# Performance work log

Hardware: AMD Instinct MI355X
Metric: run time of the kernel (lower is better)

The kernel has to match this reference:

```python
import jax, jax.numpy as jnp
import numpy as np

D = 1024      # input_dim
H = 4096      # hidden_dim
E = 8         # expert_count
TOP_K = 2
N = 8192      # tokens
LN_EPS = 1e-5


def setup_inputs() -> dict:
    key = jax.random.key(0)
    ks = jax.random.split(key, 10)
    s_d = 1.0 / np.sqrt(D)
    s_h = 1.0 / np.sqrt(H)
    return {
        "x": jax.random.normal(ks[0], (N, D), dtype=jnp.float32),
        "ln_gamma": jnp.ones((D,), jnp.float32),
        "ln_beta": jnp.zeros((D,), jnp.float32),
        "conf_w": jax.random.uniform(ks[1], (D, 1), jnp.float32, -s_d, s_d),
        "conf_b": jnp.zeros((1,), jnp.float32),
        "router_w": jax.random.uniform(ks[2], (D, E), jnp.float32, -s_d, s_d),
        "router_b": jnp.zeros((E,), jnp.float32),
        "w1": jax.random.uniform(ks[3], (E, D, H), jnp.float32, -s_d, s_d),
        "b1": jax.random.uniform(ks[4], (E, H), jnp.float32, -s_d, s_d),
        "w2": jax.random.uniform(ks[5], (E, H, D), jnp.float32, -s_h, s_h),
        "b2": jax.random.uniform(ks[6], (E, D), jnp.float32, -s_h, s_h),
    }


def reference(x, ln_gamma, ln_beta, conf_w, conf_b, router_w, router_b, w1, b1, w2, b2):
    # LayerNorm (torch default eps=1e-5, affine)
    mu = jnp.mean(x, axis=-1, keepdims=True)
    var = jnp.mean(jnp.square(x - mu), axis=-1, keepdims=True)
    x_norm = (x - mu) * jax.lax.rsqrt(var + LN_EPS) * ln_gamma + ln_beta

    # layer-skip confidence head
    confidence = jax.nn.sigmoid(x_norm @ conf_w + conf_b)  # [N,1]

    # router: softmax -> top-k -> renormalize selected weights
    router_probs = jax.nn.softmax(x_norm @ router_w + router_b, axis=-1)  # [N,E]
    vals, indices = jax.lax.top_k(router_probs, TOP_K)                    # [N,K]
    vals = vals / jnp.sum(vals, axis=-1, keepdims=True)

    # scatter top-k weights into dense per-expert combine weights [N,E]
    combine_w = jnp.zeros((x.shape[0], E), x.dtype).at[
        jnp.arange(x.shape[0])[:, None], indices].add(vals)

    # dispatch/combine: loop over small fixed expert count (dense compute,
    # weighted by combine_w, mathematically identical to per-token dispatch)
    combined = jnp.zeros_like(x)
    for e in range(E):
        h = jax.nn.relu(x_norm @ w1[e] + b1[e])      # [N,H]
        combined = combined + combine_w[:, e:e + 1] * (h @ w2[e] + b2[e])

    output = x + combined
    return output, confidence, x
```

## Files before the change

kernel.cpp:

```cpp
#include <hip/hip_runtime.h>
#include <hip/hip_bf16.h>

#define N_TOK 8192
#define DIM   1024
#define HID   4096
#define NEXP  8
#define CSTR  64
#define RTMAX 136
#define HROWS 16896
#define EPS   264

using bf16x8 = __attribute__((ext_vector_type(8))) short;
using f32x4  = __attribute__((ext_vector_type(4))) float;

__device__ __forceinline__ void gload_lds16(const void* g, void* l) {
  __builtin_amdgcn_global_load_lds(
      (const __attribute__((address_space(1))) unsigned int*)g,
      (__attribute__((address_space(3))) unsigned int*)l, 16, 0, 0);
}

__device__ __forceinline__ float wredsum(float v) {
#pragma unroll
  for (int off = 32; off > 0; off >>= 1) v += __shfl_xor(v, off, 64);
  return v;
}

__device__ __forceinline__ unsigned short f2bf(float f) {
  __hip_bfloat16 h = __float2bfloat16(f);
  return *reinterpret_cast<unsigned short*>(&h);
}
__device__ __forceinline__ float bf2f(unsigned short u) {
  return __uint_as_float((unsigned)u << 16);
}

__device__ __forceinline__ void transpose_body(
    const float* __restrict__ src, __hip_bfloat16* __restrict__ dst,
    int R, int C, int c0, int r0, float (*tile)[65]) {
  const int tid = threadIdx.x;
  const int tx = tid & 15, ty = tid >> 4;
#pragma unroll
  for (int k = 0; k < 4; k++) {
    const int row = ty + k * 16;
    const float4 v = *(const float4*)(src + (size_t)(r0 + row) * C + c0 + tx * 4);
    tile[row][tx * 4 + 0] = v.x; tile[row][tx * 4 + 1] = v.y;
    tile[row][tx * 4 + 2] = v.z; tile[row][tx * 4 + 3] = v.w;
  }
  __syncthreads();
#pragma unroll
  for (int k = 0; k < 4; k++) {
    const int orow = ty + k * 16;
    ushort4 st;
    st.x = f2bf(tile[tx * 4 + 0][orow]);
    st.y = f2bf(tile[tx * 4 + 1][orow]);
    st.z = f2bf(tile[tx * 4 + 2][orow]);
    st.w = f2bf(tile[tx * 4 + 3][orow]);
    *(ushort4*)((unsigned short*)dst + (size_t)(c0 + orow) * R + r0 + tx * 4) = st;
  }
}

__global__ __launch_bounds__(256) void setup_kernel(
    const float* __restrict__ x, const float* __restrict__ gamma, const float* __restrict__ beta,
    const float* __restrict__ conf_w, const float* __restrict__ conf_b,
    const float* __restrict__ rw, const float* __restrict__ rb,
    const float* __restrict__ w1, const float* __restrict__ w2,
    __hip_bfloat16* __restrict__ w1t, __hip_bfloat16* __restrict__ w2t,
    __hip_bfloat16* __restrict__ xn, float* __restrict__ out,
    int* __restrict__ counts, int* __restrict__ lists, float* __restrict__ wts,
    int2* __restrict__ idx) {
  __shared__ float tile[64][65];
  const int b = (int)blockIdx.x;
  if (b < 8192) {
    const int z = b >> 10, r = b & 1023;
    const int cx = r & 63, ry = r >> 6;
    transpose_body(w1 + (size_t)z * DIM * HID, w1t + (size_t)z * DIM * HID,
                   DIM, HID, cx * 64, ry * 64, tile);
    return;
  }
  if (b < 16384) {
    const int bb = b - 8192;
    const int z = bb >> 10, r = bb & 1023;
    const int cx = r & 15, ry = r >> 4;
    transpose_body(w2 + (size_t)z * HID * DIM, w2t + (size_t)z * HID * DIM,
                   HID, DIM, cx * 64, ry * 64, tile);
    return;
  }
  const int t = (b - 16384) * 4 + ((int)threadIdx.x >> 6);
  const int lane = threadIdx.x & 63;
  const float* xr = x + (size_t)t * DIM;

  float4 xv[4];
#pragma unroll
  for (int q = 0; q < 4; q++) xv[q] = *(const float4*)(xr + q * 256 + lane * 4);

  float s = 0.f, s2 = 0.f;
#pragma unroll
  for (int q = 0; q < 4; q++) {
    s  += xv[q].x + xv[q].y + xv[q].z + xv[q].w;
    s2 += xv[q].x * xv[q].x + xv[q].y * xv[q].y + xv[q].z * xv[q].z + xv[q].w * xv[q].w;
  }
  s = wredsum(s); s2 = wredsum(s2);
  const float mu  = s * (1.f / DIM);
  const float inv = rsqrtf(s2 * (1.f / DIM) - mu * mu + 1e-5f);

  float p[9];
#pragma unroll
  for (int e = 0; e < 9; e++) p[e] = 0.f;

#pragma unroll
  for (int q = 0; q < 4; q++) {
    const int d0 = q * 256 + lane * 4;
    const float4 g4 = *(const float4*)(gamma + d0);
    const float4 b4 = *(const float4*)(beta + d0);
    float v0 = (xv[q].x - mu) * inv * g4.x + b4.x;
    float v1 = (xv[q].y - mu) * inv * g4.y + b4.y;
    float v2 = (xv[q].z - mu) * inv * g4.z + b4.z;
    float v3 = (xv[q].w - mu) * inv * g4.w + b4.w;

    ushort4 st; st.x = f2bf(v0); st.y = f2bf(v1); st.z = f2bf(v2); st.w = f2bf(v3);
    *(ushort4*)((unsigned short*)xn + (size_t)t * DIM + d0) = st;
    *(float4*)(out + (size_t)t * DIM + d0) = xv[q];
    *(float4*)(out + (size_t)N_TOK * DIM + N_TOK + (size_t)t * DIM + d0) = xv[q];

    const float vv[4] = {v0, v1, v2, v3};
#pragma unroll
    for (int j = 0; j < 4; j++) {
      const int d = d0 + j;
      const float v = vv[j];
      p[8] += v * conf_w[d];
      const float4 r0 = *(const float4*)(rw + d * 8);
      const float4 r1 = *(const float4*)(rw + d * 8 + 4);
      p[0] += v * r0.x; p[1] += v * r0.y; p[2] += v * r0.z; p[3] += v * r0.w;
      p[4] += v * r1.x; p[5] += v * r1.y; p[6] += v * r1.z; p[7] += v * r1.w;
    }
  }
#pragma unroll
  for (int e = 0; e < 9; e++) p[e] = wredsum(p[e]);

  if (lane == 0) {
    float L[8];
#pragma unroll
    for (int e = 0; e < 8; e++) L[e] = p[e] + rb[e];
    const float cl = p[8] + conf_b[0];
    out[(size_t)N_TOK * DIM + t] = 1.f / (1.f + expf(-cl));

    float mx = L[0];
#pragma unroll
    for (int e = 1; e < 8; e++) mx = fmaxf(mx, L[e]);
    float pe[8];
#pragma unroll
    for (int e = 0; e < 8; e++) pe[e] = expf(L[e] - mx);
    int i0 = 0; float v0 = pe[0];
#pragma unroll
    for (int e = 1; e < 8; e++) if (pe[e] > v0) { v0 = pe[e]; i0 = e; }
    int i1 = -1; float v1 = -1.f;
#pragma unroll
    for (int e = 0; e < 8; e++) if (e != i0 && pe[e] > v1) { v1 = pe[e]; i1 = e; }
    const float wsum = v0 + v1;
    const float w0 = v0 / wsum, w1v = v1 / wsum;
    int p0 = atomicAdd(&counts[i0 * CSTR], 1);
    lists[i0 * N_TOK + p0] = t; wts[i0 * N_TOK + p0] = w0;
    int p1 = atomicAdd(&counts[i1 * CSTR], 1);
    lists[i1 * N_TOK + p1] = t; wts[i1 * N_TOK + p1] = w1v;
    idx[t] = make_int2((i0 << 13) | p0, (i1 << 13) | p1);
  }
}

__global__ void bases_kernel(const int* __restrict__ counts, int* __restrict__ bases,
                             int* __restrict__ meta) {
  if (threadIdx.x == 0) {
    int s = 0, r = 0;
#pragma unroll
    for (int e = 0; e < NEXP; e++) {
      bases[e] = s; meta[e] = r;
      const int c = counts[e * CSTR];
      s += c; r += (c + 127) >> 7;
    }
    meta[NEXP] = r;
  }
}


#define LGKM_SB(N)                                                            \
  asm volatile("s_waitcnt lgkmcnt(" #N ")" ::: "memory");                     \
  __builtin_amdgcn_sched_barrier(0);

#define MFMA_G(MI, N0, NN)                                                    \
  __builtin_amdgcn_s_setprio(1);                                              \
  _Pragma("unroll")                                                           \
  for (int n = (N0); n < (N0) + (NN); n++)                                    \
    acc[MI][n] = __builtin_amdgcn_mfma_f32_16x16x32_bf16(afr[MI], bfr[n], acc[MI][n], 0, 0, 0); \
  __builtin_amdgcn_s_setprio(0);

#define GEMM_CORE(NT)                                                                   \
  f32x4 acc[4][4] = {};                                                                 \
  stage(0, 0); stage(1, 24576);                                                         \
  for (int t = 0; t < (NT); ++t) {                                                      \
    const int pb = (t % 3) * 24576;                                                     \
    if (t + 1 < (NT)) { asm volatile("s_waitcnt vmcnt(3)" ::: "memory"); }              \
    else              { asm volatile("s_waitcnt vmcnt(0)" ::: "memory"); }              \
    __builtin_amdgcn_s_barrier();                                                       \
    if (t + 2 < (NT)) stage(t + 2, ((t + 2) % 3) * 24576);                              \
    const char* Ab = smem + pb + Abase;                                                 \
    const char* Bb = smem + pb + Bbase;                                                 \
    bf16x8 bfr[4], afr[4];                                                              \
    afr[0] = *(const bf16x8*)(Ab);                                                      \
    bfr[0] = *(const bf16x8*)(Bb);                                                      \
    bfr[1] = *(const bf16x8*)(Bb + 1024);                                               \
    __builtin_amdgcn_sched_barrier(0);                                                  \
    bfr[2] = *(const bf16x8*)(Bb + 2048);                                               \
    __builtin_amdgcn_sched_barrier(0);                                                  \
    bfr[3] = *(const bf16x8*)(Bb + 3072);                                               \
    __builtin_amdgcn_sched_barrier(0);                                                  \
    afr[1] = *(const bf16x8*)(Ab + 1024);                                               \
    __builtin_amdgcn_sched_barrier(0);                                                  \
    afr[2] = *(const bf16x8*)(Ab + 2048);                                               \
    __builtin_amdgcn_sched_barrier(0);                                                  \
    afr[3] = *(const bf16x8*)(Ab + 3072);                                               \
    __builtin_amdgcn_sched_barrier(0);                                                  \
    LGKM_SB(5) MFMA_G(0, 0, 2)                                                          \
    LGKM_SB(4) MFMA_G(0, 2, 1)                                                          \
    LGKM_SB(3) MFMA_G(0, 3, 1)                                                          \
    LGKM_SB(2) MFMA_G(1, 0, 4)                                                          \
    LGKM_SB(1) MFMA_G(2, 0, 4)                                                          \
    LGKM_SB(0) MFMA_G(3, 0, 4)                                                          \
  }

#define DECODE_TAIL()                                                         \
  if (rtg >= meta[NEXP]) return;                                              \
  int e = 0;                                                                  \
  _Pragma("unroll")                                                           \
  for (int k = 1; k < NEXP; k++) if (meta[k] <= rtg) e = k;                   \
  const int rt = rtg - meta[e];                                               \
  const int cnt = counts[e * CSTR];                                           \
  const int hbase = bases[e];

#define GEMM_COMMON()                                                         \
  __shared__ char smem[73728];                                                \
  const int tid = threadIdx.x;                                                \
  const int l = tid & 63;                                                     \
  const int w8 = tid >> 6;                                                    \
  const int wr = w8 >> 2;                                                     \
  const int wc = w8 & 3;                                                      \
  const int lr = l & 15;                                                      \
  const int pchunk = (l >> 4) ^ ((lr >> 1) & 3);                              \
  const int Abase = (wr * 64 + lr) * 64 + pchunk * 16;                        \
  const int Bbase = 8192 + (wc * 64 + lr) * 64 + pchunk * 16;                 \
  const int srow = tid >> 2;                                                  \
  const int lc = (tid & 3) ^ ((srow >> 1) & 3);

#define EPILOGUE(DSTROW)                                                      \
  __builtin_amdgcn_s_barrier();                                               \
  {                                                                           \
    unsigned short* ep = (unsigned short*)smem;                               \
    _Pragma("unroll")                                                         \
    for (int n = 0; n < 4; n++) {                                             \
      const int col = wc * 64 + n * 16 + lr;                                  \
      _Pragma("unroll")                                                       \
      for (int m = 0; m < 4; m++) {                                           \
        f32x4 v = acc[m][n];                                                  \
        _Pragma("unroll")                                                     \
        for (int j = 0; j < 4; j++) {                                         \
          const int row = wr * 64 + m * 16 + (l >> 4) * 4 + j;                \
          ep[row * EPS + col] = f2bf(v[j]);                                   \
        }                                                                     \
      }                                                                       \
    }                                                                         \
    asm volatile("s_waitcnt lgkmcnt(0)" ::: "memory");                        \
    __builtin_amdgcn_s_barrier();                                             \
    const int g = tid >> 5, u = tid & 31;                                     \
    _Pragma("unroll")                                                         \
    for (int i = 0; i < 8; i++) {                                             \
      const int row = i * 16 + g;                                             \
      const int pos = rt * 128 + row;                                         \
      if (pos < cnt) {                                                        \
        bf16x8 vv = *(const bf16x8*)(ep + row * EPS + u * 8);                 \
        *(bf16x8*)(DSTROW + u * 8) = vv;                                      \
      }                                                                       \
    }                                                                         \
  }

__global__ __launch_bounds__(512, 4) void gemm1_kernel(
    const __hip_bfloat16* __restrict__ xn, const __hip_bfloat16* __restrict__ w1t_b,
    const float* __restrict__ b1, const int* __restrict__ lists,
    const int* __restrict__ counts, const int* __restrict__ bases,
    const int* __restrict__ meta, __hip_bfloat16* __restrict__ hbuf) {
  const int x_ = (int)blockIdx.x & 7;
  const int q_ = (int)blockIdx.x >> 3;
  const int rtg = q_ >> 1;
  const int panel = x_ * 2 + (q_ & 1);
  DECODE_TAIL()
  const int ct = panel;
  const int* list = lists + e * N_TOK;
  const __hip_bfloat16* w1t = w1t_b + (size_t)e * DIM * HID;
  GEMM_COMMON()

  const int apos = rt * 128 + srow;
  const int tok = list[apos < cnt ? apos : 0];
  const unsigned short* srcA0 = (const unsigned short*)xn + (size_t)tok * DIM + lc * 8;
  const unsigned short* srcB0 = (const unsigned short*)w1t + (size_t)(ct * 256 + srow) * DIM + lc * 8;
  const unsigned short* srcB1 = (const unsigned short*)w1t + (size_t)(ct * 256 + 128 + srow) * DIM + lc * 8;

  auto stage = [&](int tt, int lbase) {
    gload_lds16(srcA0 + tt * 32, smem + lbase + tid * 16);
    gload_lds16(srcB0 + tt * 32, smem + lbase + 8192 + tid * 16);
    gload_lds16(srcB1 + tt * 32, smem + lbase + 16384 + tid * 16);
  };

  GEMM_CORE(DIM / 32)

  const float bv[4] = {
    b1[e * HID + ct * 256 + wc * 64 + 0 * 16 + lr],
    b1[e * HID + ct * 256 + wc * 64 + 1 * 16 + lr],
    b1[e * HID + ct * 256 + wc * 64 + 2 * 16 + lr],
    b1[e * HID + ct * 256 + wc * 64 + 3 * 16 + lr]};
#pragma unroll
  for (int n = 0; n < 4; n++)
#pragma unroll
    for (int m = 0; m < 4; m++)
#pragma unroll
      for (int j = 0; j < 4; j++) acc[m][n][j] = fmaxf(acc[m][n][j] + bv[n], 0.f);
  EPILOGUE((unsigned short*)hbuf + (size_t)(hbase + pos) * HID + ct * 256)
}

__global__ __launch_bounds__(512, 4) void gemm2_kernel(
    const __hip_bfloat16* __restrict__ hbuf, const __hip_bfloat16* __restrict__ w2t_b,
    const int* __restrict__ counts, const int* __restrict__ bases,
    const int* __restrict__ meta, __hip_bfloat16* __restrict__ ybuf, const int SK) {
  int panel, rtg;
  if (SK == 2) {
    const int x_ = (int)blockIdx.x & 7;
    const int q_ = (int)blockIdx.x >> 3;
    rtg = (q_ >> 2) * 4 + (x_ >> 1);
    panel = (x_ & 1) * 4 + (q_ & 3);
  } else {
    panel = (int)blockIdx.x / RTMAX;
    rtg = (int)blockIdx.x - panel * RTMAX;
  }
  DECODE_TAIL()
  const int ct = panel & 3;
  const int ksp = panel >> 2;
  const int kbase = ksp * (HID / SK);
  const __hip_bfloat16* w2t = w2t_b + (size_t)e * DIM * HID;
  GEMM_COMMON()

  const unsigned short* srcA0 = (const unsigned short*)hbuf +
      (size_t)(hbase + rt * 128 + srow) * HID + kbase + lc * 8;
  const unsigned short* srcB0 = (const unsigned short*)w2t +
      (size_t)(ct * 256 + srow) * HID + kbase + lc * 8;
  const unsigned short* srcB1 = (const unsigned short*)w2t +
      (size_t)(ct * 256 + 128 + srow) * HID + kbase + lc * 8;

  auto stage = [&](int tt, int lbase) {
    gload_lds16(srcA0 + tt * 32, smem + lbase + tid * 16);
    gload_lds16(srcB0 + tt * 32, smem + lbase + 8192 + tid * 16);
    gload_lds16(srcB1 + tt * 32, smem + lbase + 16384 + tid * 16);
  };

  const int nk = (HID / 32) / SK;
  GEMM_CORE(nk)

  EPILOGUE((unsigned short*)ybuf + ((size_t)ksp * HROWS + hbase + pos) * DIM + ct * 256)
}

__global__ __launch_bounds__(256) void combine_kernel(
    const __hip_bfloat16* __restrict__ ybuf, const float* __restrict__ b2,
    const int2* __restrict__ idx, const float* __restrict__ wv,
    const int* __restrict__ bases, float* __restrict__ out, const int SK) {
  const int t = blockIdx.x * 4 + (threadIdx.x >> 6);
  const int lane = threadIdx.x & 63;
  const int2 iv = idx[t];
  const int e0 = iv.x >> 13, p0 = iv.x & (N_TOK - 1);
  const int e1 = iv.y >> 13, p1 = iv.y & (N_TOK - 1);
  const float w0 = wv[iv.x], w1 = wv[iv.y];
  const int r0 = bases[e0] + p0;
  const int r1 = bases[e1] + p1;
#pragma unroll
  for (int q = 0; q < 4; q++) {
    const int d0 = q * 256 + lane * 4;
    float4 o = *(const float4*)(out + (size_t)t * DIM + d0);
    float y0x = 0.f, y0y = 0.f, y0z = 0.f, y0w = 0.f;
    float y1x = 0.f, y1y = 0.f, y1z = 0.f, y1w = 0.f;
    for (int s = 0; s < SK; s++) {
      const ushort4 a = *(const ushort4*)((const unsigned short*)ybuf +
                          ((size_t)s * HROWS + r0) * DIM + d0);
      const ushort4 b = *(const ushort4*)((const unsigned short*)ybuf +
                          ((size_t)s * HROWS + r1) * DIM + d0);
      y0x += bf2f(a.x); y0y += bf2f(a.y); y0z += bf2f(a.z); y0w += bf2f(a.w);
      y1x += bf2f(b.x); y1y += bf2f(b.y); y1z += bf2f(b.z); y1w += bf2f(b.w);
    }
    const float4 bb0 = *(const float4*)(b2 + e0 * DIM + d0);
    const float4 bb1 = *(const float4*)(b2 + e1 * DIM + d0);
    o.x += w0 * (y0x + bb0.x) + w1 * (y1x + bb1.x);
    o.y += w0 * (y0y + bb0.y) + w1 * (y1y + bb1.y);
    o.z += w0 * (y0z + bb0.z) + w1 * (y1z + bb1.z);
    o.w += w0 * (y0w + bb0.w) + w1 * (y1w + bb1.w);
    *(float4*)(out + (size_t)t * DIM + d0) = o;
  }
}

extern "C" void kernel_launch(void* const* d_in, const int* in_sizes, int n_in,
                              void* d_out, int out_size, void* d_ws, size_t ws_size,
                              hipStream_t stream) {
  (void)in_sizes; (void)n_in; (void)out_size;
  const float* x      = (const float*)d_in[0];
  const float* gamma  = (const float*)d_in[1];
  const float* beta   = (const float*)d_in[2];
  const float* conf_w = (const float*)d_in[3];
  const float* conf_b = (const float*)d_in[4];
  const float* rw     = (const float*)d_in[5];
  const float* rb     = (const float*)d_in[6];
  const float* w1     = (const float*)d_in[7];
  const float* b1     = (const float*)d_in[8];
  const float* w2     = (const float*)d_in[9];
  const float* b2     = (const float*)d_in[10];
  float* out = (float*)d_out;

  char* w = (char*)d_ws;
  auto alloc = [&](size_t bytes) { char* p = w; w += (bytes + 255) & ~255ULL; return p; };

  __hip_bfloat16* xn = (__hip_bfloat16*)alloc((size_t)N_TOK * DIM * 2);
  int*   lists  = (int*)alloc((size_t)NEXP * N_TOK * 4);
  float* wtsb   = (float*)alloc((size_t)NEXP * N_TOK * 4);
  int*   counts = (int*)alloc(NEXP * CSTR * 4);
  int*   bases  = (int*)alloc(256);
  int*   meta   = (int*)alloc(256);
  int2*  idx    = (int2*)alloc((size_t)N_TOK * 8);

  const size_t hbufA = (size_t)HROWS * HID * 2;
  const size_t wtA   = (size_t)NEXP * DIM * HID * 2;
  __hip_bfloat16* hbuf = (__hip_bfloat16*)alloc(hbufA);
  __hip_bfloat16* w1t  = (__hip_bfloat16*)alloc(wtA);
  __hip_bfloat16* w2t  = (__hip_bfloat16*)alloc(wtA);
  const size_t used = (size_t)(w - (char*)d_ws);
  const size_t ybuf1 = (size_t)HROWS * DIM * 2;

  int SK;
  __hip_bfloat16* ybuf;
  if (ws_size >= used + 2 * ybuf1 + 4096) {
    SK = 2; ybuf = (__hip_bfloat16*)alloc(2 * ybuf1);
  } else {
    SK = 1; ybuf = w1t;
  }
  const int g2grid = (SK == 2) ? 8 * RTMAX : 4 * RTMAX;

  hipMemsetAsync(counts, 0, NEXP * CSTR * 4, stream);
  setup_kernel<<<16384 + N_TOK / 4, 256, 0, stream>>>(
      x, gamma, beta, conf_w, conf_b, rw, rb, w1, w2, w1t, w2t,
      xn, out, counts, lists, wtsb, idx);
  bases_kernel<<<1, 64, 0, stream>>>(counts, bases, meta);
  gemm1_kernel<<<8 * 2 * RTMAX, 512, 0, stream>>>(xn, w1t, b1, lists, counts, bases, meta,
                                                  hbuf);
  gemm2_kernel<<<g2grid, 512, 0, stream>>>(hbuf, w2t, counts, bases, meta, ybuf, SK);
  combine_kernel<<<N_TOK / 4, 256, 0, stream>>>(ybuf, b2, idx, wtsb, bases, out, SK);
}
```

Measured before the change: 487.2 us.

## Use 4-wave blocks with 128x64 per-wave tiles in expert GEMMs

```diff
diff --git a/kernel.cpp b/kernel.cpp
--- a/kernel.cpp
+++ b/kernel.cpp
@@ -184,45 +184,45 @@
   asm volatile("s_waitcnt lgkmcnt(" #N ")" ::: "memory");                     \
   __builtin_amdgcn_sched_barrier(0);
 
-#define MFMA_G(MI, N0, NN)                                                    \
+#define MFMA_G(MI)                                                            \
   __builtin_amdgcn_s_setprio(1);                                              \
   _Pragma("unroll")                                                           \
-  for (int n = (N0); n < (N0) + (NN); n++)                                    \
+  for (int n = 0; n < 4; n++)                                                 \
     acc[MI][n] = __builtin_amdgcn_mfma_f32_16x16x32_bf16(afr[MI], bfr[n], acc[MI][n], 0, 0, 0); \
   __builtin_amdgcn_s_setprio(0);
 
 #define GEMM_CORE(NT)                                                                   \
-  f32x4 acc[4][4] = {};                                                                 \
+  f32x4 acc[8][4] = {};                                                                 \
   stage(0, 0); stage(1, 24576);                                                         \
   for (int t = 0; t < (NT); ++t) {                                                      \
     const int pb = (t % 3) * 24576;                                                     \
-    if (t + 1 < (NT)) { asm volatile("s_waitcnt vmcnt(3)" ::: "memory"); }              \
+    if (t + 1 < (NT)) { asm volatile("s_waitcnt vmcnt(6)" ::: "memory"); }              \
     else              { asm volatile("s_waitcnt vmcnt(0)" ::: "memory"); }              \
     __builtin_amdgcn_s_barrier();                                                       \
     if (t + 2 < (NT)) stage(t + 2, ((t + 2) % 3) * 24576);                              \
     const char* Ab = smem + pb + Abase;                                                 \
     const char* Bb = smem + pb + Bbase;                                                 \
-    bf16x8 bfr[4], afr[4];                                                              \
+    bf16x8 bfr[4], afr[8];                                                              \
     afr[0] = *(const bf16x8*)(Ab);                                                      \
     bfr[0] = *(const bf16x8*)(Bb);                                                      \
     bfr[1] = *(const bf16x8*)(Bb + 1024);                                               \
     __builtin_amdgcn_sched_barrier(0);                                                  \
     bfr[2] = *(const bf16x8*)(Bb + 2048);                                               \
-    __builtin_amdgcn_sched_barrier(0);                                                  \
     bfr[3] = *(const bf16x8*)(Bb + 3072);                                               \
     __builtin_amdgcn_sched_barrier(0);                                                  \
-    afr[1] = *(const bf16x8*)(Ab + 1024);                                               \
-    __builtin_amdgcn_sched_barrier(0);                                                  \
-    afr[2] = *(const bf16x8*)(Ab + 2048);                                               \
-    __builtin_amdgcn_sched_barrier(0);                                                  \
-    afr[3] = *(const bf16x8*)(Ab + 3072);                                               \
-    __builtin_amdgcn_sched_barrier(0);                                                  \
-    LGKM_SB(5) MFMA_G(0, 0, 2)                                                          \
-    LGKM_SB(4) MFMA_G(0, 2, 1)                                                          \
-    LGKM_SB(3) MFMA_G(0, 3, 1)                                                          \
-    LGKM_SB(2) MFMA_G(1, 0, 4)                                                          \
-    LGKM_SB(1) MFMA_G(2, 0, 4)                                                          \
-    LGKM_SB(0) MFMA_G(3, 0, 4)                                                          \
+    _Pragma("unroll")                                                                   \
+    for (int m = 1; m < 8; m++) {                                                       \
+      afr[m] = *(const bf16x8*)(Ab + m * 1024);                                         \
+      __builtin_amdgcn_sched_barrier(0);                                                \
+    }                                                                                   \
+    LGKM_SB(7) MFMA_G(0)                                                                \
+    LGKM_SB(6) MFMA_G(1)                                                                \
+    LGKM_SB(5) MFMA_G(2)                                                                \
+    LGKM_SB(4) MFMA_G(3)                                                                \
+    LGKM_SB(3) MFMA_G(4)                                                                \
+    LGKM_SB(2) MFMA_G(5)                                                                \
+    LGKM_SB(1) MFMA_G(6)                                                                \
+    LGKM_SB(0) MFMA_G(7)                                                                \
   }
 
 #define DECODE_TAIL()                                                         \
@@ -236,16 +236,14 @@
 
 #define GEMM_COMMON()                                                         \
   __shared__ char smem[73728];                                                \
-  const int tid = threadIdx.x;                                                \
+  const int tid = threadIdx.x;                     \
   const int l = tid & 63;                                                     \
-  const int w8 = tid >> 6;                                                    \
-  const int wr = w8 >> 2;                                                     \
-  const int wc = w8 & 3;                                                      \
+  const int wc = tid >> 6;                                                    \
   const int lr = l & 15;                                                      \
   const int pchunk = (l >> 4) ^ ((lr >> 1) & 3);                              \
-  const int Abase = (wr * 64 + lr) * 64 + pchunk * 16;                        \
+  const int Abase = lr * 64 + pchunk * 16;                                    \
   const int Bbase = 8192 + (wc * 64 + lr) * 64 + pchunk * 16;                 \
-  const int srow = tid >> 2;                                                  \
+  const int srow = tid >> 2;                       \
   const int lc = (tid & 3) ^ ((srow >> 1) & 3);
 
 #define EPILOGUE(DSTROW)                                                      \
@@ -256,11 +254,11 @@
     for (int n = 0; n < 4; n++) {                                             \
       const int col = wc * 64 + n * 16 + lr;                                  \
       _Pragma("unroll")                                                       \
-      for (int m = 0; m < 4; m++) {                                           \
+      for (int m = 0; m < 8; m++) {                                           \
         f32x4 v = acc[m][n];                                                  \
         _Pragma("unroll")                                                     \
         for (int j = 0; j < 4; j++) {                                         \
-          const int row = wr * 64 + m * 16 + (l >> 4) * 4 + j;                \
+          const int row = m * 16 + (l >> 4) * 4 + j;                          \
           ep[row * EPS + col] = f2bf(v[j]);                                   \
         }                                                                     \
       }                                                                       \
@@ -269,8 +267,8 @@
     __builtin_amdgcn_s_barrier();                                             \
     const int g = tid >> 5, u = tid & 31;                                     \
     _Pragma("unroll")                                                         \
-    for (int i = 0; i < 8; i++) {                                             \
-      const int row = i * 16 + g;                                             \
+    for (int i = 0; i < 16; i++) {                                            \
+      const int row = i * 8 + g;                                              \
       const int pos = rt * 128 + row;                                         \
       if (pos < cnt) {                                                        \
         bf16x8 vv = *(const bf16x8*)(ep + row * EPS + u * 8);                 \
@@ -279,7 +277,7 @@
     }                                                                         \
   }
 
-__global__ __launch_bounds__(512, 4) void gemm1_kernel(
+__global__ __launch_bounds__(256, 2) void gemm1_kernel(
     const __hip_bfloat16* __restrict__ xn, const __hip_bfloat16* __restrict__ w1t_b,
     const float* __restrict__ b1, const int* __restrict__ lists,
     const int* __restrict__ counts, const int* __restrict__ bases,
@@ -294,16 +292,23 @@
   const __hip_bfloat16* w1t = w1t_b + (size_t)e * DIM * HID;
   GEMM_COMMON()
 
-  const int apos = rt * 128 + srow;
-  const int tok = list[apos < cnt ? apos : 0];
-  const unsigned short* srcA0 = (const unsigned short*)xn + (size_t)tok * DIM + lc * 8;
+  const int ap0 = rt * 128 + srow, ap1 = ap0 + 64;
+  const int tok0 = list[ap0 < cnt ? ap0 : 0];
+  const int tok1 = list[ap1 < cnt ? ap1 : 0];
+  const unsigned short* srcA0 = (const unsigned short*)xn + (size_t)tok0 * DIM + lc * 8;
+  const unsigned short* srcA1 = (const unsigned short*)xn + (size_t)tok1 * DIM + lc * 8;
   const unsigned short* srcB0 = (const unsigned short*)w1t + (size_t)(ct * 256 + srow) * DIM + lc * 8;
-  const unsigned short* srcB1 = (const unsigned short*)w1t + (size_t)(ct * 256 + 128 + srow) * DIM + lc * 8;
+  const unsigned short* srcB1 = (const unsigned short*)w1t + (size_t)(ct * 256 + 64 + srow) * DIM + lc * 8;
+  const unsigned short* srcB2 = (const unsigned short*)w1t + (size_t)(ct * 256 + 128 + srow) * DIM + lc * 8;
+  const unsigned short* srcB3 = (const unsigned short*)w1t + (size_t)(ct * 256 + 192 + srow) * DIM + lc * 8;
 
   auto stage = [&](int tt, int lbase) {
     gload_lds16(srcA0 + tt * 32, smem + lbase + tid * 16);
+    gload_lds16(srcA1 + tt * 32, smem + lbase + 4096 + tid * 16);
     gload_lds16(srcB0 + tt * 32, smem + lbase + 8192 + tid * 16);
-    gload_lds16(srcB1 + tt * 32, smem + lbase + 16384 + tid * 16);
+    gload_lds16(srcB1 + tt * 32, smem + lbase + 12288 + tid * 16);
+    gload_lds16(srcB2 + tt * 32, smem + lbase + 16384 + tid * 16);
+    gload_lds16(srcB3 + tt * 32, smem + lbase + 20480 + tid * 16);
   };
 
   GEMM_CORE(DIM / 32)
@@ -316,13 +321,13 @@
 #pragma unroll
   for (int n = 0; n < 4; n++)
 #pragma unroll
-    for (int m = 0; m < 4; m++)
+    for (int m = 0; m < 8; m++)
 #pragma unroll
       for (int j = 0; j < 4; j++) acc[m][n][j] = fmaxf(acc[m][n][j] + bv[n], 0.f);
   EPILOGUE((unsigned short*)hbuf + (size_t)(hbase + pos) * HID + ct * 256)
 }
 
-__global__ __launch_bounds__(512, 4) void gemm2_kernel(
+__global__ __launch_bounds__(256, 2) void gemm2_kernel(
     const __hip_bfloat16* __restrict__ hbuf, const __hip_bfloat16* __restrict__ w2t_b,
     const int* __restrict__ counts, const int* __restrict__ bases,
     const int* __restrict__ meta, __hip_bfloat16* __restrict__ ybuf, const int SK) {
@@ -345,15 +350,24 @@
 
   const unsigned short* srcA0 = (const unsigned short*)hbuf +
       (size_t)(hbase + rt * 128 + srow) * HID + kbase + lc * 8;
+  const unsigned short* srcA1 = (const unsigned short*)hbuf +
+      (size_t)(hbase + rt * 128 + 64 + srow) * HID + kbase + lc * 8;
   const unsigned short* srcB0 = (const unsigned short*)w2t +
       (size_t)(ct * 256 + srow) * HID + kbase + lc * 8;
   const unsigned short* srcB1 = (const unsigned short*)w2t +
+      (size_t)(ct * 256 + 64 + srow) * HID + kbase + lc * 8;
+  const unsigned short* srcB2 = (const unsigned short*)w2t +
       (size_t)(ct * 256 + 128 + srow) * HID + kbase + lc * 8;
+  const unsigned short* srcB3 = (const unsigned short*)w2t +
+      (size_t)(ct * 256 + 192 + srow) * HID + kbase + lc * 8;
 
   auto stage = [&](int tt, int lbase) {
     gload_lds16(srcA0 + tt * 32, smem + lbase + tid * 16);
+    gload_lds16(srcA1 + tt * 32, smem + lbase + 4096 + tid * 16);
     gload_lds16(srcB0 + tt * 32, smem + lbase + 8192 + tid * 16);
-    gload_lds16(srcB1 + tt * 32, smem + lbase + 16384 + tid * 16);
+    gload_lds16(srcB1 + tt * 32, smem + lbase + 12288 + tid * 16);
+    gload_lds16(srcB2 + tt * 32, smem + lbase + 16384 + tid * 16);
+    gload_lds16(srcB3 + tt * 32, smem + lbase + 20480 + tid * 16);
   };
 
   const int nk = (HID / 32) / SK;
@@ -448,8 +462,8 @@
       x, gamma, beta, conf_w, conf_b, rw, rb, w1, w2, w1t, w2t,
       xn, out, counts, lists, wtsb, idx);
   bases_kernel<<<1, 64, 0, stream>>>(counts, bases, meta);
-  gemm1_kernel<<<8 * 2 * RTMAX, 512, 0, stream>>>(xn, w1t, b1, lists, counts, bases, meta,
+  gemm1_kernel<<<8 * 2 * RTMAX, 256, 0, stream>>>(xn, w1t, b1, lists, counts, bases, meta,
                                                   hbuf);
-  gemm2_kernel<<<g2grid, 512, 0, stream>>>(hbuf, w2t, counts, bases, meta, ybuf, SK);
+  gemm2_kernel<<<g2grid, 256, 0, stream>>>(hbuf, w2t, counts, bases, meta, ybuf, SK);
   combine_kernel<<<N_TOK / 4, 256, 0, stream>>>(ybuf, b2, idx, wtsb, bases, out, SK);
 }
```

Measured after the change: 487.0 us. No clear change (-0.0%).
